# Kernel tuning notes

Measured on AMD Instinct MI355X. Metric: run time of the kernel, lower is better.

The kernel has to match this reference:

```python
import jax, jax.numpy as jnp
import numpy as np

N = 30000      # nodes
NNZ = 480000   # edges (avg degree 16)
D_IN, D_H, D_OUT = 64, 256, 128


def spmm(rows, cols, vals, feat, n):
    # (sparse [n,n] in COO) @ feat : out[r] += vals[e] * feat[cols[e]]
    return jax.ops.segment_sum(vals[:, None] * feat[cols], rows, num_segments=n)


def graph_inception(l_feat, r_feat, rows, cols, vals, W1, b1, W2, b2):
    # hop=1, eval mode (F.dropout with training=False is identity)
    n = l_feat.shape[0]
    x0 = r_feat  # dropout(Korder_list[r][0])
    x1 = l_feat  # dropout(Korder_list[l][0])
    # network_l @ x0 and network_r (=transpose) @ x1
    l_K = spmm(rows, cols, vals, x0, n)          # [N, D]
    r_K = spmm(cols, rows, vals, x1, n)          # [N, D]
    l_re = l_K @ W1 + b1                          # weight1(l_Korder)
    r_re = r_K @ W1 + b1
    # Multiply: mm(network, a) * b then weight2 (mm result equals l_K / r_K)
    l_mul = (l_K * x1) @ W2 + b2
    r_mul = (r_K * x0) @ W2 + b2
    return l_re + l_mul, r_re + r_mul


def setup_inputs() -> dict:
    key = jax.random.key(0)
    ks = jax.random.split(key, 9)
    l_feat = jax.random.normal(ks[0], (N, D_IN), jnp.float32)
    r_feat = jax.random.normal(ks[1], (N, D_IN), jnp.float32)
    edge_rows = jax.random.randint(ks[2], (NNZ,), 0, N, jnp.int32)
    edge_cols = jax.random.randint(ks[3], (NNZ,), 0, N, jnp.int32)
    edge_vals = jax.random.uniform(ks[4], (NNZ,), jnp.float32)
    W1 = jax.random.normal(ks[5], (D_IN, D_H), jnp.float32) / np.sqrt(D_IN)
    W2 = jax.random.normal(ks[6], (D_IN, D_H), jnp.float32) / np.sqrt(D_IN)
    W3 = jax.random.normal(ks[7], (D_H, D_OUT), jnp.float32) / np.sqrt(D_H)
    W4 = jax.random.normal(ks[8], (D_H, D_OUT), jnp.float32) / np.sqrt(D_H)
    return {
        "l_feat": l_feat, "r_feat": r_feat,
        "edge_rows": edge_rows, "edge_cols": edge_cols, "edge_vals": edge_vals,
        "W1": W1, "b1": jnp.zeros((D_H,), jnp.float32),
        "W2": W2, "b2": jnp.zeros((D_H,), jnp.float32),
        "W3": W3, "b3": jnp.zeros((D_OUT,), jnp.float32),
        "W4": W4, "b4": jnp.zeros((D_OUT,), jnp.float32),
    }


def reference(l_feat, r_feat, edge_rows, edge_cols, edge_vals,
              W1, b1, W2, b2, W3, b3, W4, b4):
    a1, b1_ = graph_inception(l_feat, r_feat, edge_rows, edge_cols, edge_vals, W1, b1, W2, b2)
    y1 = jax.nn.relu(a1)
    z1 = jax.nn.relu(b1_)
    a2, _ = graph_inception(y1, z1, edge_rows, edge_cols, edge_vals, W3, b3, W4, b4)
    return jax.nn.relu(a2)  # [N, 128]
```

## Files before the change

kernel.cpp:

```cpp
#include <hip/hip_runtime.h>

#define NN    30000
#define NNZE  480000
#define NPART 8
#define PROWS (NN / NPART)

using s8 = __attribute__((ext_vector_type(8))) short;
using f4 = __attribute__((ext_vector_type(4))) float;

__device__ __forceinline__ unsigned short f2bf(float x) {
    unsigned int u = __float_as_uint(x);
    u += 0x7fff + ((u >> 16) & 1);
    return (unsigned short)(u >> 16);
}
__device__ __forceinline__ float bf2f(unsigned short h) {
    return __uint_as_float(((unsigned int)h) << 16);
}
__device__ __forceinline__ float bflo(unsigned int z) {
    return __uint_as_float(z << 16);
}
__device__ __forceinline__ float bfhi(unsigned int z) {
    return __uint_as_float(z & 0xffff0000u);
}
__device__ __forceinline__ int2 nt_pair(const int2* p) {
    long long v = __builtin_nontemporal_load((const long long*)p);
    int2 r; r.x = (int)(unsigned int)v; r.y = (int)(v >> 32); return r;
}

#define FEAT4   (NN * 64 / 4)
#define PREP_W0 (2 * FEAT4)
#define PREP_W1 (PREP_W0 + 98688)
#define PREP_Z  (PREP_W1 + 2 * NN / 4)
__global__ __launch_bounds__(256) void prep_kernel(
    const float* __restrict__ lf, const float* __restrict__ rf,
    const float* __restrict__ W1, const float* __restrict__ W2,
    const float* __restrict__ W3, const float* __restrict__ W4,
    const float* __restrict__ b1, const float* __restrict__ b2,
    const float* __restrict__ b3, const float* __restrict__ b4,
    unsigned short* __restrict__ lfb, unsigned short* __restrict__ rfb,
    unsigned short* __restrict__ Wt1, unsigned short* __restrict__ Wt2,
    float* __restrict__ bias1, float* __restrict__ bias2,
    int* __restrict__ cnt)
{
    int i = blockIdx.x * 256 + threadIdx.x;
    if (i < PREP_W0) {
        const float* src = (i < FEAT4) ? lf : rf;
        unsigned short* dst = (i < FEAT4) ? lfb : rfb;
        int j = (i < FEAT4) ? i : i - FEAT4;
        float4 v = ((const float4*)src)[j];
        ushort4 o;
        o.x = f2bf(v.x); o.y = f2bf(v.y); o.z = f2bf(v.z); o.w = f2bf(v.w);
        ((ushort4*)dst)[j] = o;
    } else if (i < PREP_W1) {
        int j = i - PREP_W0;
        if (j < 32768) {
            int n = j >> 7, k = j & 127;
            float v = (k < 64) ? W1[(size_t)k * 256 + n] : W2[(size_t)(k - 64) * 256 + n];
            Wt1[j] = f2bf(v);
        } else if (j < 32768 + 65536) {
            int q = j - 32768;
            int n = q >> 9, k = q & 511;
            float v = (k < 256) ? W3[(size_t)k * 128 + n] : W4[(size_t)(k - 256) * 128 + n];
            Wt2[q] = f2bf(v);
        } else if (j < 98304 + 256) {
            int n = j - 98304; bias1[n] = b1[n] + b2[n];
        } else if (j < 98560 + 128) {
            int n = j - 98560; bias2[n] = b3[n] + b4[n];
        }
    } else if (i < PREP_Z) {
        int j = i - PREP_W1;
        ((int4*)cnt)[j] = make_int4(0, 0, 0, 0);
    }
}

__global__ __launch_bounds__(256) void histrank_kernel(
    const int* __restrict__ rows, const int* __restrict__ cols,
    int* __restrict__ rc, int* __restrict__ cc,
    int* __restrict__ rank_r, int* __restrict__ rank_c)
{
    int e = blockIdx.x * 256 + threadIdx.x;
    if (e < NNZE) {
        int r = __builtin_nontemporal_load(rows + e);
        rank_r[e] = atomicAdd(&rc[r], 1);
        int c = __builtin_nontemporal_load(cols + e);
        rank_c[e] = atomicAdd(&cc[c], 1);
    }
}

#define SCB 118
__global__ __launch_bounds__(256) void scan_local_kernel(
    const int* __restrict__ rc, const int* __restrict__ cc,
    int* __restrict__ rp, int* __restrict__ cp, int* __restrict__ totals)
{
    int b = blockIdx.x;
    const int* cnt = (b < SCB) ? rc : cc;
    int*       esc = (b < SCB) ? rp : cp;
    int lb = (b < SCB) ? b : b - SCB;
    int t = threadIdx.x;
    int idx = lb * 256 + t;

    __shared__ int s[256];
    int v = (idx < NN) ? cnt[idx] : 0;
    s[t] = v;
    __syncthreads();
#pragma unroll
    for (int off = 1; off < 256; off <<= 1) {
        int u = (t >= off) ? s[t - off] : 0;
        __syncthreads();
        s[t] += u;
        __syncthreads();
    }
    if (idx < NN) esc[idx] = s[t] - v;
    if (t == 255) totals[b] = s[t];
}

__global__ __launch_bounds__(256) void scan_addtot_kernel(
    int* __restrict__ rp, int* __restrict__ cp, const int* __restrict__ totals)
{
    int b = blockIdx.x;
    int side = (b >= SCB) ? 1 : 0;
    int lb = side ? b - SCB : b;
    int t = threadIdx.x;

    __shared__ int s[128];
    if (t < 128) s[t] = (t < SCB) ? totals[side * SCB + t] : 0;
    __syncthreads();
#pragma unroll
    for (int off = 1; off < 128; off <<= 1) {
        int u = 0;
        if (t < 128 && t >= off) u = s[t - off];
        __syncthreads();
        if (t < 128) s[t] += u;
        __syncthreads();
    }
    int off = (lb == 0) ? 0 : s[lb - 1];
    int idx = lb * 256 + t;
    int* ptr = side ? cp : rp;
    if (idx < NN) ptr[idx] += off;
    if (b == 0   && t == 0) rp[NN] = NNZE;
    if (b == SCB && t == 0) cp[NN] = NNZE;
}

__global__ __launch_bounds__(256) void scatter_rank_kernel(
    const int* __restrict__ rows, const int* __restrict__ cols,
    const float* __restrict__ vals,
    const int* __restrict__ rank_r, const int* __restrict__ rank_c,
    const int* __restrict__ rp, const int* __restrict__ cp,
    int2* __restrict__ csr_pair, int2* __restrict__ csc_pair)
{
    int part = blockIdx.x & (NPART - 1);
    int lo = part * PROWS, hi = lo + PROWS;
    int nb = gridDim.x >> 3;
    int bj = blockIdx.x >> 3;
    int stride = nb * 256;
    for (int e = bj * 256 + threadIdx.x; e < NNZE; e += stride) {
        int r = __builtin_nontemporal_load(rows + e);
        int c = __builtin_nontemporal_load(cols + e);
        float fv = __builtin_nontemporal_load(vals + e);
        int vb = __float_as_int(fv);
        if (r >= lo && r < hi) {
            int p = rp[r] + __builtin_nontemporal_load(rank_r + e);
            csr_pair[p] = make_int2(c, vb);
        }
        if (c >= lo && c < hi) {
            int q = cp[c] + __builtin_nontemporal_load(rank_c + e);
            csc_pair[q] = make_int2(r, vb);
        }
    }
}

__global__ __launch_bounds__(256) void gather64_x_kernel(
    const int* __restrict__ rp, const int2* __restrict__ rpair,
    const int* __restrict__ cp, const int2* __restrict__ cpair,
    const unsigned short* __restrict__ lfb, const unsigned short* __restrict__ rfb,
    unsigned short* __restrict__ X1, unsigned short* __restrict__ X2)
{
    int side = blockIdx.y;
    const int*  ptr  = side ? cp    : rp;
    const int2* pair = side ? cpair : rpair;
    const unsigned int* gf = (const unsigned int*)(side ? lfb : rfb);
    const unsigned int* mf = (const unsigned int*)(side ? rfb : lfb);
    unsigned int* X = (unsigned int*)(side ? X2 : X1);

    int w = blockIdx.x * 8 + (threadIdx.x >> 5);
    int l = threadIdx.x & 31;
    int e0 = ptr[w], e1 = ptr[w + 1];
    float a0 = 0.f, a1 = 0.f;
    int e = e0;
    for (; e + 7 < e1; e += 8) {
        int2 p[8];
#pragma unroll
        for (int j = 0; j < 8; ++j) p[j] = nt_pair(&pair[e + j]);
        unsigned int z[8];
#pragma unroll
        for (int j = 0; j < 8; ++j) z[j] = gf[(size_t)p[j].x * 32 + l];
#pragma unroll
        for (int j = 0; j < 8; ++j) {
            float v = __int_as_float(p[j].y);
            a0 += v * bflo(z[j]);
            a1 += v * bfhi(z[j]);
        }
    }
    for (; e < e1; ++e) {
        int2 p0 = nt_pair(&pair[e]);
        unsigned int z0 = gf[(size_t)p0.x * 32 + l];
        float v = __int_as_float(p0.y);
        a0 += v * bflo(z0);
        a1 += v * bfhi(z0);
    }
    unsigned int m = mf[(size_t)w * 32 + l];
    float m0 = a0 * bflo(m);
    float m1 = a1 * bfhi(m);
    X[(size_t)w * 64 + l]      = (unsigned int)f2bf(a0) | ((unsigned int)f2bf(a1) << 16);
    X[(size_t)w * 64 + 32 + l] = (unsigned int)f2bf(m0) | ((unsigned int)f2bf(m1) << 16);
}

__global__ __launch_bounds__(256) void gather256_x_kernel(
    const int* __restrict__ ptr, const int2* __restrict__ pair,
    const unsigned short* __restrict__ z1b, const unsigned short* __restrict__ y1b,
    unsigned short* __restrict__ X3)
{
    int w    = blockIdx.x * 4 + (threadIdx.x >> 6);
    int lane = threadIdx.x & 63;
    int e0 = ptr[w], e1 = ptr[w + 1];
    const ushort4* Z = (const ushort4*)z1b;
    f4 acc = {0.f, 0.f, 0.f, 0.f};
    int e = e0;
    for (; e + 7 < e1; e += 8) {
        int2 p[8];
#pragma unroll
        for (int j = 0; j < 8; ++j) p[j] = nt_pair(&pair[e + j]);
        ushort4 z[8];
#pragma unroll
        for (int j = 0; j < 8; ++j) z[j] = Z[(size_t)p[j].x * 64 + lane];
#pragma unroll
        for (int j = 0; j < 8; ++j) {
            float v = __int_as_float(p[j].y);
            acc[0] += v * bf2f(z[j].x);
            acc[1] += v * bf2f(z[j].y);
            acc[2] += v * bf2f(z[j].z);
            acc[3] += v * bf2f(z[j].w);
        }
    }
    for (; e < e1; ++e) {
        int2 p0 = nt_pair(&pair[e]);
        float v0 = __int_as_float(p0.y);
        ushort4 z0 = Z[(size_t)p0.x * 64 + lane];
        acc[0] += v0 * bf2f(z0.x);
        acc[1] += v0 * bf2f(z0.y);
        acc[2] += v0 * bf2f(z0.z);
        acc[3] += v0 * bf2f(z0.w);
    }
    ushort4 y = ((const ushort4*)y1b)[(size_t)w * 64 + lane];
    ushort4 o0, o1;
    o0.x = f2bf(acc[0]); o0.y = f2bf(acc[1]); o0.z = f2bf(acc[2]); o0.w = f2bf(acc[3]);
    o1.x = f2bf(acc[0] * bf2f(y.x));
    o1.y = f2bf(acc[1] * bf2f(y.y));
    o1.z = f2bf(acc[2] * bf2f(y.z));
    o1.w = f2bf(acc[3] * bf2f(y.w));
    ((ushort4*)X3)[(size_t)w * 128 + lane]      = o0;
    ((ushort4*)X3)[(size_t)w * 128 + 64 + lane] = o1;
}

template<int K, int DOUT, bool OUT_BF16>
__global__ __launch_bounds__(256) void mfma_gemm_kernel(
    const unsigned short* Xa, const unsigned short* Xb,
    const unsigned short* __restrict__ Wt, const float* __restrict__ bias,
    void* outa, void* outb)
{
    constexpr int WC = DOUT / 4;
    constexpr int FN = WC / 16;
    __shared__ s8 sX[64 * 8];
    __shared__ s8 sW[DOUT * 8];

    const unsigned short* X = blockIdx.y ? Xb : Xa;
    void* outv              = blockIdx.y ? outb : outa;

    const int t       = threadIdx.x;
    const int rowbase = blockIdx.x * 64;
    const int wid     = t >> 6;
    const int lane    = t & 63;
    const int l15     = lane & 15;
    const int kg      = lane >> 4;

    f4 acc[4][FN] = {};

    for (int kc = 0; kc < K; kc += 64) {
#pragma unroll
        for (int it = 0; it < 2; ++it) {
            int ch = t + it * 256;
            int r = ch >> 3, c = ch & 7;
            int row = rowbase + r;
            s8 v = {};
            if (row < NN) v = ((const s8*)X)[((size_t)row * K + kc) / 8 + c];
            sX[(r << 3) | (c ^ (r & 7))] = v;
        }
#pragma unroll
        for (int it = 0; it < DOUT / 32; ++it) {
            int ch = t + it * 256;
            int n = ch >> 3, c = ch & 7;
            sW[(n << 3) | (c ^ (n & 7))] = ((const s8*)Wt)[((size_t)n * K + kc) / 8 + c];
        }
        __syncthreads();

#pragma unroll
        for (int ks = 0; ks < 2; ++ks) {
            int cch = ks * 4 + kg;
            s8 a[4], b[FN];
#pragma unroll
            for (int fm = 0; fm < 4; ++fm) {
                int r0 = fm * 16 + l15;
                a[fm] = sX[(r0 << 3) | (cch ^ (r0 & 7))];
            }
#pragma unroll
            for (int fn = 0; fn < FN; ++fn) {
                int n0 = wid * WC + fn * 16 + l15;
                b[fn] = sW[(n0 << 3) | (cch ^ (n0 & 7))];
            }
#pragma unroll
            for (int fm = 0; fm < 4; ++fm)
#pragma unroll
                for (int fn = 0; fn < FN; ++fn)
                    acc[fm][fn] = __builtin_amdgcn_mfma_f32_16x16x32_bf16(
                        a[fm], b[fn], acc[fm][fn], 0, 0, 0);
        }
        __syncthreads();
    }

#pragma unroll
    for (int fm = 0; fm < 4; ++fm) {
#pragma unroll
        for (int fn = 0; fn < FN; ++fn) {
            int col = wid * WC + fn * 16 + l15;
            float bv = bias[col];
#pragma unroll
            for (int j = 0; j < 4; ++j) {
                int row = rowbase + fm * 16 + kg * 4 + j;
                if (row < NN) {
                    float v = fmaxf(acc[fm][fn][j] + bv, 0.f);
                    if constexpr (OUT_BF16)
                        ((unsigned short*)outv)[(size_t)row * DOUT + col] = f2bf(v);
                    else
                        ((float*)outv)[(size_t)row * DOUT + col] = v;
                }
            }
        }
    }
}

extern "C" void kernel_launch(void* const* d_in, const int* in_sizes, int n_in,
                              void* d_out, int out_size, void* d_ws, size_t ws_size,
                              hipStream_t stream)
{
    const float* l_feat = (const float*)d_in[0];
    const float* r_feat = (const float*)d_in[1];
    const int*   rows   = (const int*)  d_in[2];
    const int*   cols   = (const int*)  d_in[3];
    const float* vals   = (const float*)d_in[4];
    const float* W1     = (const float*)d_in[5];
    const float* b1     = (const float*)d_in[6];
    const float* W2     = (const float*)d_in[7];
    const float* b2     = (const float*)d_in[8];
    const float* W3     = (const float*)d_in[9];
    const float* b3     = (const float*)d_in[10];
    const float* W4     = (const float*)d_in[11];
    const float* b4     = (const float*)d_in[12];
    float* out = (float*)d_out;

    char* p = (char*)d_ws;
    unsigned short* X1  = (unsigned short*)p; p += (size_t)NN * 128 * 2;
    unsigned short* X2  = (unsigned short*)p; p += (size_t)NN * 128 * 2;
    unsigned short* X3  = (unsigned short*)p; p += (size_t)NN * 512 * 2;
    unsigned short* z1b = (unsigned short*)p; p += (size_t)NN * 256 * 2;
    unsigned short* y1b = (unsigned short*)p; p += (size_t)NN * 256 * 2;
    unsigned short* lfb = (unsigned short*)p; p += (size_t)NN * 64 * 2;
    unsigned short* rfb = (unsigned short*)p; p += (size_t)NN * 64 * 2;
    int* row_cnt  = (int*)p; p += (size_t)NN * 4;
    int* col_cnt  = (int*)p; p += (size_t)NN * 4;
    int* totals   = (int*)p; p += 256 * 4;
    unsigned short* Wt1 = (unsigned short*)p; p += 32768 * 2;
    unsigned short* Wt2 = (unsigned short*)p; p += 65536 * 2;
    float* bias1 = (float*)p; p += 256 * 4;
    float* bias2 = (float*)p; p += 128 * 4;
    int*   row_ptr  = (int*)p; p += (size_t)(NN + 4) * 4;
    int*   col_ptr  = (int*)p; p += (size_t)(NN + 4) * 4;
    int2*  csr_pair = (int2*)p; p += (size_t)NNZE * 8;
    int2*  csc_pair = (int2*)p; p += (size_t)NNZE * 8;
    int*   rank_r   = (int*)p; p += (size_t)NNZE * 4;
    int*   rank_c   = (int*)p; p += (size_t)NNZE * 4;

    prep_kernel<<<(PREP_Z + 255) / 256, 256, 0, stream>>>(
        l_feat, r_feat, W1, W2, W3, W4, b1, b2, b3, b4,
        lfb, rfb, Wt1, Wt2, bias1, bias2, row_cnt);

    histrank_kernel<<<(NNZE + 255) / 256, 256, 0, stream>>>(
        rows, cols, row_cnt, col_cnt, rank_r, rank_c);

    scan_local_kernel<<<2 * SCB, 256, 0, stream>>>(row_cnt, col_cnt, row_ptr, col_ptr, totals);
    scan_addtot_kernel<<<2 * SCB, 256, 0, stream>>>(row_ptr, col_ptr, totals);

    scatter_rank_kernel<<<1024, 256, 0, stream>>>(
        rows, cols, vals, rank_r, rank_c, row_ptr, col_ptr, csr_pair, csc_pair);

    {
        dim3 grid(NN / 8, 2);
        gather64_x_kernel<<<grid, 256, 0, stream>>>(
            row_ptr, csr_pair, col_ptr, csc_pair, lfb, rfb, X1, X2);
    }

    {
        dim3 grid((NN + 63) / 64, 2);
        mfma_gemm_kernel<128, 256, true><<<grid, 256, 0, stream>>>(
            X1, X2, Wt1, bias1, y1b, z1b);
    }

    gather256_x_kernel<<<NN / 4, 256, 0, stream>>>(row_ptr, csr_pair, z1b, y1b, X3);

    {
        dim3 grid((NN + 63) / 64, 1);
        mfma_gemm_kernel<512, 128, false><<<grid, 256, 0, stream>>>(
            X3, X3, Wt2, bias2, out, out);
    }
}
```

Measured before the change: 199.7 us.

## Replace global atomic histogram with per-chunk LDS histograms and chunk-offset scan

Replaces the global-atomic per-edge counting with 128 blocks that each build a shared-memory histogram over half the bins for one edge chunk. Each block writes per-chunk counts, and the scan kernel first turns those counts into exclusive per-chunk offsets before the usual block scan. Ranks shrink to 16-bit, and the scatter adds a per-chunk offset read. This removes contended global atomics and the count-zeroing pass. In exchange it adds a 7.7 MB partial-histogram buffer, strided column reads in the scan, and only 128 blocks of parallelism for counting.

```diff
diff --git a/kernel.cpp b/kernel.cpp
--- a/kernel.cpp
+++ b/kernel.cpp
@@ -1,9 +1,13 @@
 #include <hip/hip_runtime.h>
 
-#define NN    30000
-#define NNZE  480000
-#define NPART 8
-#define PROWS (NN / NPART)
+#define NN     30000
+#define NNZE   480000
+#define NPART  8
+#define PROWS  (NN / NPART)
+#define NCHUNK 32
+#define CH_E   (NNZE / NCHUNK)
+#define HBIN   (NN / 2)
+#define SCB    118
 
 using s8 = __attribute__((ext_vector_type(8))) short;
 using f4 = __attribute__((ext_vector_type(4))) float;
@@ -30,7 +34,6 @@
 #define FEAT4   (NN * 64 / 4)
 #define PREP_W0 (2 * FEAT4)
 #define PREP_W1 (PREP_W0 + 98688)
-#define PREP_Z  (PREP_W1 + 2 * NN / 4)
 __global__ __launch_bounds__(256) void prep_kernel(
     const float* __restrict__ lf, const float* __restrict__ rf,
     const float* __restrict__ W1, const float* __restrict__ W2,
@@ -39,8 +42,7 @@
     const float* __restrict__ b3, const float* __restrict__ b4,
     unsigned short* __restrict__ lfb, unsigned short* __restrict__ rfb,
     unsigned short* __restrict__ Wt1, unsigned short* __restrict__ Wt2,
-    float* __restrict__ bias1, float* __restrict__ bias2,
-    int* __restrict__ cnt)
+    float* __restrict__ bias1, float* __restrict__ bias2)
 {
     int i = blockIdx.x * 256 + threadIdx.x;
     if (i < PREP_W0) {
@@ -67,41 +69,61 @@
         } else if (j < 98560 + 128) {
             int n = j - 98560; bias2[n] = b3[n] + b4[n];
         }
-    } else if (i < PREP_Z) {
-        int j = i - PREP_W1;
-        ((int4*)cnt)[j] = make_int4(0, 0, 0, 0);
-    }
-}
-
-__global__ __launch_bounds__(256) void histrank_kernel(
+    }
+}
+
+__global__ __launch_bounds__(256) void count_rank_kernel(
     const int* __restrict__ rows, const int* __restrict__ cols,
-    int* __restrict__ rc, int* __restrict__ cc,
-    int* __restrict__ rank_r, int* __restrict__ rank_c)
-{
-    int e = blockIdx.x * 256 + threadIdx.x;
-    if (e < NNZE) {
-        int r = __builtin_nontemporal_load(rows + e);
-        rank_r[e] = atomicAdd(&rc[r], 1);
-        int c = __builtin_nontemporal_load(cols + e);
-        rank_c[e] = atomicAdd(&cc[c], 1);
-    }
-}
-
-#define SCB 118
-__global__ __launch_bounds__(256) void scan_local_kernel(
-    const int* __restrict__ rc, const int* __restrict__ cc,
+    int* __restrict__ histP,
+    unsigned short* __restrict__ rank_r, unsigned short* __restrict__ rank_c)
+{
+    int b = blockIdx.x;
+    int side  = b >> 6;
+    int chunk = (b & 63) >> 1;
+    int half  = b & 1;
+    const int* keys = side ? cols : rows;
+    unsigned short* rank = side ? rank_c : rank_r;
+    int binlo = half * HBIN;
+
+    __shared__ int h[HBIN];
+    for (int i = threadIdx.x; i < HBIN; i += 256) h[i] = 0;
+    __syncthreads();
+
+    int e0 = chunk * CH_E;
+    for (int e = e0 + threadIdx.x; e < e0 + CH_E; e += 256) {
+        int k = __builtin_nontemporal_load(keys + e) - binlo;
+        if ((unsigned)k < (unsigned)HBIN)
+            rank[e] = (unsigned short)atomicAdd(&h[k], 1);
+    }
+    __syncthreads();
+
+    int* dst = histP + ((size_t)(side * NCHUNK + chunk)) * NN + binlo;
+    for (int i = threadIdx.x; i < HBIN; i += 256)
+        __builtin_nontemporal_store(h[i], dst + i);
+}
+
+__global__ __launch_bounds__(256) void scanP_kernel(
+    int* __restrict__ histP,
     int* __restrict__ rp, int* __restrict__ cp, int* __restrict__ totals)
 {
     int b = blockIdx.x;
-    const int* cnt = (b < SCB) ? rc : cc;
-    int*       esc = (b < SCB) ? rp : cp;
-    int lb = (b < SCB) ? b : b - SCB;
+    int side = (b >= SCB) ? 1 : 0;
+    int lb = side ? b - SCB : b;
     int t = threadIdx.x;
-    int idx = lb * 256 + t;
-
+    int bin = lb * 256 + t;
+
+    int run = 0;
+    if (bin < NN) {
+        int* base = histP + (size_t)side * NCHUNK * NN + bin;
+#pragma unroll 4
+        for (int c = 0; c < NCHUNK; ++c) {
+            int v = base[(size_t)c * NN];
+            base[(size_t)c * NN] = run;
+            run += v;
+        }
+    }
     __shared__ int s[256];
-    int v = (idx < NN) ? cnt[idx] : 0;
-    s[t] = v;
+    s[t] = run;
     __syncthreads();
 #pragma unroll
     for (int off = 1; off < 256; off <<= 1) {
@@ -110,7 +132,7 @@
         s[t] += u;
         __syncthreads();
     }
-    if (idx < NN) esc[idx] = s[t] - v;
+    if (bin < NN) (side ? cp : rp)[bin] = s[t] - run;
     if (t == 255) totals[b] = s[t];
 }
 
@@ -144,7 +166,8 @@
 __global__ __launch_bounds__(256) void scatter_rank_kernel(
     const int* __restrict__ rows, const int* __restrict__ cols,
     const float* __restrict__ vals,
-    const int* __restrict__ rank_r, const int* __restrict__ rank_c,
+    const unsigned short* __restrict__ rank_r, const unsigned short* __restrict__ rank_c,
+    const int* __restrict__ histP,
     const int* __restrict__ rp, const int* __restrict__ cp,
     int2* __restrict__ csr_pair, int2* __restrict__ csc_pair)
 {
@@ -158,12 +181,15 @@
         int c = __builtin_nontemporal_load(cols + e);
         float fv = __builtin_nontemporal_load(vals + e);
         int vb = __float_as_int(fv);
+        int chunk = e / CH_E;
         if (r >= lo && r < hi) {
-            int p = rp[r] + __builtin_nontemporal_load(rank_r + e);
+            int p = rp[r] + histP[(size_t)chunk * NN + r]
+                  + (int)__builtin_nontemporal_load(rank_r + e);
             csr_pair[p] = make_int2(c, vb);
         }
         if (c >= lo && c < hi) {
-            int q = cp[c] + __builtin_nontemporal_load(rank_c + e);
+            int q = cp[c] + histP[(size_t)(NCHUNK + chunk) * NN + c]
+                  + (int)__builtin_nontemporal_load(rank_c + e);
             csc_pair[q] = make_int2(r, vb);
         }
     }
@@ -375,8 +401,7 @@
     unsigned short* y1b = (unsigned short*)p; p += (size_t)NN * 256 * 2;
     unsigned short* lfb = (unsigned short*)p; p += (size_t)NN * 64 * 2;
     unsigned short* rfb = (unsigned short*)p; p += (size_t)NN * 64 * 2;
-    int* row_cnt  = (int*)p; p += (size_t)NN * 4;
-    int* col_cnt  = (int*)p; p += (size_t)NN * 4;
+    int* histP    = (int*)p; p += (size_t)2 * NCHUNK * NN * 4;
     int* totals   = (int*)p; p += 256 * 4;
     unsigned short* Wt1 = (unsigned short*)p; p += 32768 * 2;
     unsigned short* Wt2 = (unsigned short*)p; p += 65536 * 2;
@@ -386,21 +411,20 @@
     int*   col_ptr  = (int*)p; p += (size_t)(NN + 4) * 4;
     int2*  csr_pair = (int2*)p; p += (size_t)NNZE * 8;
     int2*  csc_pair = (int2*)p; p += (size_t)NNZE * 8;
-    int*   rank_r   = (int*)p; p += (size_t)NNZE * 4;
-    int*   rank_c   = (int*)p; p += (size_t)NNZE * 4;
-
-    prep_kernel<<<(PREP_Z + 255) / 256, 256, 0, stream>>>(
+    unsigned short* rank_r = (unsigned short*)p; p += (size_t)NNZE * 2;
+    unsigned short* rank_c = (unsigned short*)p; p += (size_t)NNZE * 2;
+
+    prep_kernel<<<(PREP_W1 + 255) / 256, 256, 0, stream>>>(
         l_feat, r_feat, W1, W2, W3, W4, b1, b2, b3, b4,
-        lfb, rfb, Wt1, Wt2, bias1, bias2, row_cnt);
-
-    histrank_kernel<<<(NNZE + 255) / 256, 256, 0, stream>>>(
-        rows, cols, row_cnt, col_cnt, rank_r, rank_c);
-
-    scan_local_kernel<<<2 * SCB, 256, 0, stream>>>(row_cnt, col_cnt, row_ptr, col_ptr, totals);
+        lfb, rfb, Wt1, Wt2, bias1, bias2);
+
+    count_rank_kernel<<<128, 256, 0, stream>>>(rows, cols, histP, rank_r, rank_c);
+
+    scanP_kernel<<<2 * SCB, 256, 0, stream>>>(histP, row_ptr, col_ptr, totals);
     scan_addtot_kernel<<<2 * SCB, 256, 0, stream>>>(row_ptr, col_ptr, totals);
 
     scatter_rank_kernel<<<1024, 256, 0, stream>>>(
-        rows, cols, vals, rank_r, rank_c, row_ptr, col_ptr, csr_pair, csc_pair);
+        rows, cols, vals, rank_r, rank_c, histP, row_ptr, col_ptr, csr_pair, csc_pair);
 
     {
         dim3 grid(NN / 8, 2);
```

Result: no change. 198.5 us (-0.6%).
